# Kernel optimization log

Measured on AMD Instinct MI355X. Metric: run time of the kernel, lower is better.

## Reference

```python
import jax, jax.numpy as jnp
import numpy as np

HID = 256
VOC = 50257
N_E_SH = 2
N_E_SP = 2
N_MB = 4
B, S = 8, 512
LN_EPS = 1e-3  # keras LayerNormalization default epsilon
STD = 0.02


def setup_inputs() -> dict:
    key = jax.random.key(0)
    ks = jax.random.split(key, 10)
    x = jax.random.normal(ks[0], (B, S, HID), dtype=jnp.float32)
    # labels drawn in [1, VOC) so the `labels > 0` mask keeps every token (static shape)
    labels = jax.random.randint(ks[1], (B, S), 1, VOC, dtype=jnp.int32)
    xb = jax.random.randint(ks[2], (B, S), 0, N_MB + 1, dtype=jnp.int32)
    W_sh = jax.random.normal(ks[3], (N_E_SH, HID, HID), dtype=jnp.float32) * STD
    b_sh = jax.random.normal(ks[4], (N_E_SH, HID), dtype=jnp.float32) * STD
    W_sp = jax.random.normal(ks[5], (N_MB * N_E_SP, HID, HID), dtype=jnp.float32) * STD
    b_sp = jax.random.normal(ks[6], (N_MB * N_E_SP, HID), dtype=jnp.float32) * STD
    w_gates = jax.random.normal(ks[7], (N_MB, HID, N_E_SH + N_E_SP), dtype=jnp.float32) * STD
    vocab_bias = jax.random.normal(ks[8], (VOC,), dtype=jnp.float32) * STD
    emb = jax.random.normal(ks[9], (VOC, HID), dtype=jnp.float32) * STD  # tied_to.weights[0]
    ln_gamma = jnp.ones((HID,), dtype=jnp.float32)
    ln_beta = jnp.zeros((HID,), dtype=jnp.float32)
    return {"x": x, "labels": labels, "xb": xb, "W_sh": W_sh, "b_sh": b_sh,
            "W_sp": W_sp, "b_sp": b_sp, "w_gates": w_gates,
            "vocab_bias": vocab_bias, "emb": emb,
            "ln_gamma": ln_gamma, "ln_beta": ln_beta}


def _layernorm(h, gamma, beta):
    mu = jnp.mean(h, axis=-1, keepdims=True)
    var = jnp.mean(jnp.square(h - mu), axis=-1, keepdims=True)
    return gamma * (h - mu) * jax.lax.rsqrt(var + LN_EPS) + beta


def reference(x, labels, xb, W_sh, b_sh, W_sp, b_sp, w_gates, vocab_bias, emb, ln_gamma, ln_beta):
    xf = x.reshape(-1, HID)          # [N, H]
    lf = labels.reshape(-1)          # [N], all > 0 => mask gather is identity
    xbf = xb.reshape(-1)             # [N]

    # shared + branch-specific experts: [e, N, H]
    sh = jnp.einsum('nd,edh->enh', xf, W_sh) + b_sh[:, None, :]
    sp = jnp.einsum('nd,edh->enh', xf, W_sp) + b_sp[:, None, :]
    sp = sp.reshape(N_MB, N_E_SP, -1, HID)                       # [t, e_sp, N, H]
    sh_b = jnp.broadcast_to(sh[None], (N_MB, N_E_SH, sh.shape[1], HID))
    merge = jnp.concatenate([sh_b, sp], axis=1)                  # [t, e, N, H]

    gates = jax.nn.softmax(jnp.einsum('nd,tde->tne', xf, w_gates), axis=-1)  # [t, N, e]
    out = jnp.einsum('tend,tne->tnd', merge, gates)              # [t, N, H]

    outputs = jnp.concatenate([jnp.zeros_like(xf)[None], out], axis=0)  # [t+1, N, H]
    oh = jax.nn.one_hot(xbf, N_MB + 1, dtype=jnp.float32)        # [N, t+1]
    e_out = jnp.einsum('tnd,nt->nd', outputs, oh)                # [N, H]

    e_out = _layernorm(e_out, ln_gamma, ln_beta) + xf

    logits = e_out @ emb.T + vocab_bias                          # [N, VOC]
    logp = jax.nn.log_softmax(logits, axis=-1)
    loss = -jnp.take_along_axis(logp, lf[:, None], axis=-1)[:, 0]  # [N]
    prob = jnp.exp(logp)
    return prob, loss
```

## Files before the change

kernel.cpp:

```cpp
#include <hip/hip_runtime.h>

#define HID 256
#define VOC 50257
#define NTOK 4096
#define NCT3 393
#define CG 8
#define TN 128
#define LN_EPS 1e-3f
#define PROB_ELEMS 205852672

typedef __attribute__((ext_vector_type(8))) short bf16x8;
typedef __attribute__((ext_vector_type(4))) float f32x4;
typedef __attribute__((ext_vector_type(16))) float f32x16;

__device__ inline unsigned short f2bf(float f) {
    unsigned int u = __builtin_bit_cast(unsigned int, f);
    unsigned int r = u + 0x7FFFu + ((u >> 16) & 1u);
    return (unsigned short)(r >> 16);
}
__device__ inline float bf2f(unsigned short b) {
    unsigned int u = ((unsigned int)b) << 16;
    return __builtin_bit_cast(float, u);
}

__global__ void conv_f32_bf16(const float* __restrict__ src,
                              unsigned short* __restrict__ dst, int n4) {
    int i = blockIdx.x * blockDim.x + threadIdx.x;
    int stride = gridDim.x * blockDim.x;
    for (; i < n4; i += stride) {
        float4 v = reinterpret_cast<const float4*>(src)[i];
        ushort4 o;
        o.x = f2bf(v.x); o.y = f2bf(v.y); o.z = f2bf(v.z); o.w = f2bf(v.w);
        reinterpret_cast<ushort4*>(dst)[i] = o;
    }
}

__global__ __launch_bounds__(256) void wt_transpose(
    const float* __restrict__ Wsh, const float* __restrict__ Wsp,
    unsigned short* __restrict__ Wtbf) {
    __shared__ float t[64][65];
    int gcol0 = blockIdx.x * 64;
    int k0 = blockIdx.y * 64;
    int e = gcol0 >> 8, h0 = gcol0 & 255;
    const float* Wp = (e < 2) ? (Wsh + e * 65536) : (Wsp + (e - 2) * 65536);
    int tid = threadIdx.x;
#pragma unroll
    for (int i = 0; i < 16; ++i) {
        int id = tid + i * 256;
        int k = id >> 6, h = id & 63;
        t[k][h] = Wp[(k0 + k) * 256 + h0 + h];
    }
    __syncthreads();
#pragma unroll
    for (int i = 0; i < 4; ++i) {
        int id = tid + i * 256;
        int h = id >> 4, kq = id & 15;
        ushort4 o;
        o.x = f2bf(t[kq * 4 + 0][h]); o.y = f2bf(t[kq * 4 + 1][h]);
        o.z = f2bf(t[kq * 4 + 2][h]); o.w = f2bf(t[kq * 4 + 3][h]);
        *reinterpret_cast<ushort4*>(Wtbf + (size_t)(gcol0 + h) * 256 + k0 + kq * 4) = o;
    }
}

__global__ __launch_bounds__(256) void expert_gemm(
    const unsigned short* __restrict__ xbf,
    const unsigned short* __restrict__ Wtbf,
    const float* __restrict__ bsh, const float* __restrict__ bsp,
    float* __restrict__ cexp) {
    __shared__ unsigned short sA[64 * 256];
    __shared__ unsigned short sB[128 * 256];
    int bid = blockIdx.x;
    int rt = bid & 63;
    int ct = bid >> 6;
    int row0 = rt * 64, col0 = ct * 128;
    int tid = threadIdx.x;

#pragma unroll
    for (int i = 0; i < 8; ++i) {
        int id = tid + i * 256;
        int r = id >> 5, c = id & 31;
        bf16x8 v = *reinterpret_cast<const bf16x8*>(xbf + (row0 + r) * 256 + c * 8);
        *reinterpret_cast<bf16x8*>(sA + r * 256 + ((c ^ (r & 7)) * 8)) = v;
    }
#pragma unroll
    for (int i = 0; i < 16; ++i) {
        int id = tid + i * 256;
        int j = id >> 5, c = id & 31;
        bf16x8 v = *reinterpret_cast<const bf16x8*>(Wtbf + (size_t)(col0 + j) * 256 + c * 8);
        *reinterpret_cast<bf16x8*>(sB + j * 256 + ((c ^ (j & 7)) * 8)) = v;
    }
    __syncthreads();

    int lane = tid & 63, wave = tid >> 6;
    int wcol = wave * 32;
    int lrow = lane & 15, g = lane >> 4;
    f32x4 zero4 = {0.f, 0.f, 0.f, 0.f};
    f32x4 acc[4][2];
#pragma unroll
    for (int mf = 0; mf < 4; ++mf)
#pragma unroll
        for (int nf = 0; nf < 2; ++nf) acc[mf][nf] = zero4;

#pragma unroll
    for (int ks = 0; ks < 8; ++ks) {
        int kc = ks * 4 + g;
        bf16x8 a[4], b[2];
#pragma unroll
        for (int mf = 0; mf < 4; ++mf) {
            int r = mf * 16 + lrow;
            a[mf] = *reinterpret_cast<const bf16x8*>(sA + r * 256 + ((kc ^ (r & 7)) * 8));
        }
#pragma unroll
        for (int nf = 0; nf < 2; ++nf) {
            int j = wcol + nf * 16 + lrow;
            b[nf] = *reinterpret_cast<const bf16x8*>(sB + j * 256 + ((kc ^ (j & 7)) * 8));
        }
#pragma unroll
        for (int mf = 0; mf < 4; ++mf)
#pragma unroll
            for (int nf = 0; nf < 2; ++nf)
                acc[mf][nf] = __builtin_amdgcn_mfma_f32_16x16x32_bf16(a[mf], b[nf], acc[mf][nf], 0, 0, 0);
    }

#pragma unroll
    for (int nf = 0; nf < 2; ++nf) {
        int col = col0 + wcol + nf * 16 + lrow;
        int e = col >> 8, h = col & 255;
        float bias = (e < 2) ? bsh[e * 256 + h] : bsp[(e - 2) * 256 + h];
#pragma unroll
        for (int mf = 0; mf < 4; ++mf)
#pragma unroll
            for (int r = 0; r < 4; ++r) {
                int row = row0 + mf * 16 + g * 4 + r;
                cexp[(size_t)row * 2560 + col] = acc[mf][nf][r] + bias;
            }
    }
}

__global__ __launch_bounds__(256) void combine_ln(
    const float* __restrict__ x, const int* __restrict__ xb,
    const float* __restrict__ wg, const float* __restrict__ cexp,
    const float* __restrict__ gamma, const float* __restrict__ beta,
    unsigned short* __restrict__ ebf) {
    __shared__ float sx[256];
    __shared__ float sg[4];
    __shared__ float rs[4], rq[4];
    int n = blockIdx.x, h = threadIdx.x;
    float xv = x[n * 256 + h];
    sx[h] = xv;
    __syncthreads();
    int xbn = xb[n];
    float eo;
    if (xbn == 0) {
        eo = beta[h] + xv;
    } else {
        int t = xbn - 1;
        int wv = h >> 6, lane = h & 63;
        float p = 0.f;
        const float* wgt = wg + t * 1024;
#pragma unroll
        for (int i = 0; i < 4; ++i) {
            int d = lane * 4 + i;
            p += sx[d] * wgt[d * 4 + wv];
        }
#pragma unroll
        for (int off = 32; off; off >>= 1) p += __shfl_down(p, off);
        if (lane == 0) sg[wv] = p;
        __syncthreads();
        float g0 = sg[0], g1 = sg[1], g2 = sg[2], g3 = sg[3];
        float mx = fmaxf(fmaxf(g0, g1), fmaxf(g2, g3));
        float e0 = __expf(g0 - mx), e1 = __expf(g1 - mx);
        float e2 = __expf(g2 - mx), e3 = __expf(g3 - mx);
        float inv = 1.f / (e0 + e1 + e2 + e3);
        const float* cr = cexp + (size_t)n * 2560;
        float o = (e0 * cr[h] + e1 * cr[256 + h] +
                   e2 * cr[512 + t * 512 + h] + e3 * cr[768 + t * 512 + h]) * inv;
        float s = o, q = o * o;
#pragma unroll
        for (int off = 32; off; off >>= 1) { s += __shfl_down(s, off); q += __shfl_down(q, off); }
        if (lane == 0) { rs[wv] = s; rq[wv] = q; }
        __syncthreads();
        float mu = (rs[0] + rs[1] + rs[2] + rs[3]) * (1.f / 256.f);
        float ex2 = (rq[0] + rq[1] + rq[2] + rq[3]) * (1.f / 256.f);
        float var = ex2 - mu * mu;
        eo = gamma[h] * (o - mu) * rsqrtf(var + LN_EPS) + beta[h] + xv;
    }
    ebf[n * 256 + h] = f2bf(eo);
}

template <int PASS>
__global__ __launch_bounds__(512, 2) void big_gemm(
    const unsigned short* __restrict__ ebf,
    const unsigned short* __restrict__ embbf,
    const float* __restrict__ vbias,
    float* __restrict__ psum,
    const float* __restrict__ denom,
    float* __restrict__ prob) {
    __shared__ unsigned short sB[2][TN * 256];

    int bid = blockIdx.x;
    int rt = bid >> 3;
    int cg = bid & 7;
    int row0 = rt * 128;
    int tid = threadIdx.x;
    int wave = tid >> 6, lane = tid & 63;
    int l31 = lane & 31, hi = lane >> 5;
    int wr = wave >> 2, wc = wave & 3;
    int nmy = (NCT3 - cg + CG - 1) / CG;

    bf16x8 a[2][16];
    {
        const unsigned short* ab =
            ebf + (size_t)(row0 + wr * 64 + l31) * 256 + hi * 8;
#pragma unroll
        for (int mf = 0; mf < 2; ++mf)
#pragma unroll
            for (int ks = 0; ks < 16; ++ks)
                a[mf][ks] = *reinterpret_cast<const bf16x8*>(ab + mf * 32 * 256 + ks * 16);
    }

    auto stage = [&](int ct, int buf) {
        int col0 = ct * TN;
#pragma unroll
        for (int i = 0; i < 8; ++i) {
            int col = i * 16 + wave * 2 + hi;
            int gcol = col0 + col; if (gcol >= VOC) gcol = VOC - 1;
            const unsigned short* src =
                embbf + (size_t)gcol * 256 + ((l31 ^ (col & 7)) * 8);
            unsigned short* dst = (unsigned short*)sB[buf] + (size_t)(i * 512 + wave * 64) * 8;
            __builtin_amdgcn_global_load_lds(
                (const __attribute__((address_space(1))) void*)src,
                (__attribute__((address_space(3))) void*)dst, 16, 0, 0);
        }
    };

    stage(cg, 0);
    asm volatile("s_waitcnt vmcnt(0)" ::: "memory");
    __syncthreads();

    float invd[2][16];
    if (PASS == 1) {
#pragma unroll
        for (int mf = 0; mf < 2; ++mf)
#pragma unroll
            for (int r = 0; r < 16; ++r) {
                int row = row0 + wr * 64 + mf * 32 + (r & 3) + 8 * (r >> 2) + 4 * hi;
                invd[mf][r] = 1.f / denom[row];
            }
    }
    float es[2][16];
    if (PASS == 0) {
#pragma unroll
        for (int mf = 0; mf < 2; ++mf)
#pragma unroll
            for (int r = 0; r < 16; ++r) es[mf][r] = 0.f;
    }

    f32x16 zz = {0.f,0.f,0.f,0.f,0.f,0.f,0.f,0.f,0.f,0.f,0.f,0.f,0.f,0.f,0.f,0.f};

    for (int it = 0; it < nmy; ++it) {
        int ct = cg + it * CG;
        if (it + 1 < nmy) stage(ct + CG, (it + 1) & 1);

        int gc = ct * TN + wc * 32 + l31;
        float bvb;
        if (PASS == 0) bvb = (gc < VOC) ? vbias[gc] : -1e4f;
        else           bvb = vbias[(gc < VOC) ? gc : (VOC - 1)];

        const unsigned short* sBc = (const unsigned short*)sB[it & 1];
        int bcol = wc * 32 + l31;
        f32x16 c0 = zz, c1 = zz;
#pragma unroll
        for (int ks = 0; ks < 16; ++ks) {
            int kc = ks * 2 + hi;
            bf16x8 b = *reinterpret_cast<const bf16x8*>(
                sBc + bcol * 256 + ((kc ^ (bcol & 7)) * 8));
            c0 = __builtin_amdgcn_mfma_f32_32x32x16_bf16(a[0][ks], b, c0, 0, 0, 0);
            c1 = __builtin_amdgcn_mfma_f32_32x32x16_bf16(a[1][ks], b, c1, 0, 0, 0);
        }

        asm volatile("s_waitcnt vmcnt(0)" ::: "memory");
        __syncthreads();

        if (PASS == 0) {
#pragma unroll
            for (int r = 0; r < 16; ++r) {
                es[0][r] += __expf(c0[r] + bvb);
                es[1][r] += __expf(c1[r] + bvb);
            }
        } else {
            if (gc < VOC) {
#pragma unroll
                for (int r = 0; r < 16; ++r) {
                    int rowr = row0 + wr * 64 + (r & 3) + 8 * (r >> 2) + 4 * hi;
                    prob[(size_t)rowr * VOC + gc] = __expf(c0[r] + bvb) * invd[0][r];
                    prob[(size_t)(rowr + 32) * VOC + gc] = __expf(c1[r] + bvb) * invd[1][r];
                }
            }
        }
    }

    if (PASS == 0) {
#pragma unroll
        for (int mf = 0; mf < 2; ++mf)
#pragma unroll
            for (int r = 0; r < 16; ++r) {
                float v = es[mf][r];
#pragma unroll
                for (int off = 1; off < 32; off <<= 1) v += __shfl_xor(v, off);
                if (l31 == 0) {
                    int row = row0 + wr * 64 + mf * 32 + (r & 3) + 8 * (r >> 2) + 4 * hi;
                    psum[(size_t)row * 32 + cg * 4 + wc] = v;
                }
            }
    }
}

__global__ __launch_bounds__(64) void finalize_k(
    const float* __restrict__ psum,
    const unsigned short* __restrict__ ebf, const unsigned short* __restrict__ embbf,
    const float* __restrict__ vbias, const int* __restrict__ labels,
    float* __restrict__ denom, float* __restrict__ loss) {
    int n = blockIdx.x, lane = threadIdx.x;
    float s = (lane < 32) ? psum[(size_t)n * 32 + lane] : 0.f;
#pragma unroll
    for (int off = 1; off < 32; off <<= 1) s += __shfl_xor(s, off);
    int lf = labels[n];
    const unsigned short* ev = ebf + n * 256;
    const unsigned short* mv = embbf + (size_t)lf * 256;
    float p = 0.f;
#pragma unroll
    for (int i = 0; i < 4; ++i) p += bf2f(ev[lane * 4 + i]) * bf2f(mv[lane * 4 + i]);
#pragma unroll
    for (int off = 1; off < 64; off <<= 1) p += __shfl_xor(p, off);
    if (lane == 0) {
        denom[n] = s;
        loss[n] = logf(s) - (p + vbias[lf]);
    }
}

extern "C" void kernel_launch(void* const* d_in, const int* in_sizes, int n_in,
                              void* d_out, int out_size, void* d_ws, size_t ws_size,
                              hipStream_t stream) {
    const float* x      = (const float*)d_in[0];
    const int*   labels = (const int*)d_in[1];
    const int*   xb     = (const int*)d_in[2];
    const float* Wsh    = (const float*)d_in[3];
    const float* bsh    = (const float*)d_in[4];
    const float* Wsp    = (const float*)d_in[5];
    const float* bsp    = (const float*)d_in[6];
    const float* wg     = (const float*)d_in[7];
    const float* vbias  = (const float*)d_in[8];
    const float* emb    = (const float*)d_in[9];
    const float* gamma  = (const float*)d_in[10];
    const float* beta   = (const float*)d_in[11];

    char* ws = (char*)d_ws;
    unsigned short* xbf   = (unsigned short*)(ws + 0);
    unsigned short* embbf = (unsigned short*)(ws + 2097152);
    unsigned short* Wtbf  = (unsigned short*)(ws + 27828736);
    float* cexp           = (float*)(ws + 29360128);
    unsigned short* ebf   = (unsigned short*)(ws + 71303168);
    float* psum           = (float*)(ws + 73400320);
    float* denom          = (float*)(ws + 73924608);

    float* prob = (float*)d_out;
    float* loss = prob + PROB_ELEMS;

    conv_f32_bf16<<<dim3(512), dim3(256), 0, stream>>>(x, xbf, NTOK * HID / 4);
    conv_f32_bf16<<<dim3(2048), dim3(256), 0, stream>>>(emb, embbf, VOC * HID / 4);
    wt_transpose<<<dim3(40, 4), dim3(256), 0, stream>>>(Wsh, Wsp, Wtbf);
    expert_gemm<<<dim3(64 * 20), dim3(256), 0, stream>>>(xbf, Wtbf, bsh, bsp, cexp);
    combine_ln<<<dim3(NTOK), dim3(256), 0, stream>>>(x, xb, wg, cexp, gamma, beta, ebf);
    big_gemm<0><<<dim3(256), dim3(512), 0, stream>>>(ebf, embbf, vbias, psum, nullptr, nullptr);
    finalize_k<<<dim3(NTOK), dim3(64), 0, stream>>>(psum, ebf, embbf, vbias, labels, denom, loss);
    big_gemm<1><<<dim3(256), dim3(512), 0, stream>>>(ebf, embbf, vbias, nullptr, denom, prob);
}
```

Baseline: 540.1 us.

## Merge prep kernels, fuse x conversion into expert GEMM, shrink expert tile

Combines the emb bf16 conversion and the weight transpose into a single prep kernel, removing two launches. The expert GEMM now reads fp32 x directly and converts it to bf16 while staging into shared memory, which drops the separate x conversion pass. The expert GEMM column tile shrinks from 128 to 64, doubling the grid and cutting shared memory per block for better occupancy. In exchange each x tile is read and converted twice as many times, and each wave issues fewer MFMAs per A-fragment load.

Result: no change. 533.5 us (-1.2%).

```diff
diff --git a/kernel.cpp b/kernel.cpp
--- a/kernel.cpp
+++ b/kernel.cpp
@@ -23,67 +23,76 @@
     return __builtin_bit_cast(float, u);
 }
 
-__global__ void conv_f32_bf16(const float* __restrict__ src,
-                              unsigned short* __restrict__ dst, int n4) {
-    int i = blockIdx.x * blockDim.x + threadIdx.x;
-    int stride = gridDim.x * blockDim.x;
-    for (; i < n4; i += stride) {
-        float4 v = reinterpret_cast<const float4*>(src)[i];
-        ushort4 o;
-        o.x = f2bf(v.x); o.y = f2bf(v.y); o.z = f2bf(v.z); o.w = f2bf(v.w);
-        reinterpret_cast<ushort4*>(dst)[i] = o;
-    }
-}
-
-__global__ __launch_bounds__(256) void wt_transpose(
-    const float* __restrict__ Wsh, const float* __restrict__ Wsp,
-    unsigned short* __restrict__ Wtbf) {
+__global__ __launch_bounds__(256) void prep_kernel(
+    const float* __restrict__ emb, const float* __restrict__ Wsh,
+    const float* __restrict__ Wsp,
+    unsigned short* __restrict__ embbf, unsigned short* __restrict__ Wtbf) {
     __shared__ float t[64][65];
-    int gcol0 = blockIdx.x * 64;
-    int k0 = blockIdx.y * 64;
-    int e = gcol0 >> 8, h0 = gcol0 & 255;
-    const float* Wp = (e < 2) ? (Wsh + e * 65536) : (Wsp + (e - 2) * 65536);
     int tid = threadIdx.x;
-#pragma unroll
-    for (int i = 0; i < 16; ++i) {
-        int id = tid + i * 256;
-        int k = id >> 6, h = id & 63;
-        t[k][h] = Wp[(k0 + k) * 256 + h0 + h];
-    }
-    __syncthreads();
-#pragma unroll
-    for (int i = 0; i < 4; ++i) {
-        int id = tid + i * 256;
-        int h = id >> 4, kq = id & 15;
-        ushort4 o;
-        o.x = f2bf(t[kq * 4 + 0][h]); o.y = f2bf(t[kq * 4 + 1][h]);
-        o.z = f2bf(t[kq * 4 + 2][h]); o.w = f2bf(t[kq * 4 + 3][h]);
-        *reinterpret_cast<ushort4*>(Wtbf + (size_t)(gcol0 + h) * 256 + k0 + kq * 4) = o;
+    if (blockIdx.x < 160) {
+        int bx = blockIdx.x % 40, by = blockIdx.x / 40;
+        int gcol0 = bx * 64;
+        int k0 = by * 64;
+        int e = gcol0 >> 8, h0 = gcol0 & 255;
+        const float* Wp = (e < 2) ? (Wsh + e * 65536) : (Wsp + (e - 2) * 65536);
+#pragma unroll
+        for (int i = 0; i < 16; ++i) {
+            int id = tid + i * 256;
+            int k = id >> 6, h = id & 63;
+            t[k][h] = Wp[(k0 + k) * 256 + h0 + h];
+        }
+        __syncthreads();
+#pragma unroll
+        for (int i = 0; i < 4; ++i) {
+            int id = tid + i * 256;
+            int h = id >> 4, kq = id & 15;
+            ushort4 o;
+            o.x = f2bf(t[kq * 4 + 0][h]); o.y = f2bf(t[kq * 4 + 1][h]);
+            o.z = f2bf(t[kq * 4 + 2][h]); o.w = f2bf(t[kq * 4 + 3][h]);
+            *reinterpret_cast<ushort4*>(Wtbf + (size_t)(gcol0 + h) * 256 + k0 + kq * 4) = o;
+        }
+    } else {
+        const int n4 = VOC * HID / 4;
+        int i = (blockIdx.x - 160) * 256 + tid;
+        int stride = (gridDim.x - 160) * 256;
+        for (; i < n4; i += stride) {
+            float4 v = reinterpret_cast<const float4*>(emb)[i];
+            ushort4 o;
+            o.x = f2bf(v.x); o.y = f2bf(v.y); o.z = f2bf(v.z); o.w = f2bf(v.w);
+            reinterpret_cast<ushort4*>(embbf)[i] = o;
+        }
     }
 }
 
 __global__ __launch_bounds__(256) void expert_gemm(
-    const unsigned short* __restrict__ xbf,
+    const float* __restrict__ x,
     const unsigned short* __restrict__ Wtbf,
     const float* __restrict__ bsh, const float* __restrict__ bsp,
     float* __restrict__ cexp) {
     __shared__ unsigned short sA[64 * 256];
-    __shared__ unsigned short sB[128 * 256];
+    __shared__ unsigned short sB[64 * 256];
     int bid = blockIdx.x;
     int rt = bid & 63;
     int ct = bid >> 6;
-    int row0 = rt * 64, col0 = ct * 128;
+    int row0 = rt * 64, col0 = ct * 64;
     int tid = threadIdx.x;
 
 #pragma unroll
     for (int i = 0; i < 8; ++i) {
         int id = tid + i * 256;
         int r = id >> 5, c = id & 31;
-        bf16x8 v = *reinterpret_cast<const bf16x8*>(xbf + (row0 + r) * 256 + c * 8);
-        *reinterpret_cast<bf16x8*>(sA + r * 256 + ((c ^ (r & 7)) * 8)) = v;
-    }
-#pragma unroll
-    for (int i = 0; i < 16; ++i) {
+        const float* xr = x + (size_t)(row0 + r) * 256 + c * 8;
+        float4 v0 = *reinterpret_cast<const float4*>(xr);
+        float4 v1 = *reinterpret_cast<const float4*>(xr + 4);
+        bf16x8 o;
+        o[0] = (short)f2bf(v0.x); o[1] = (short)f2bf(v0.y);
+        o[2] = (short)f2bf(v0.z); o[3] = (short)f2bf(v0.w);
+        o[4] = (short)f2bf(v1.x); o[5] = (short)f2bf(v1.y);
+        o[6] = (short)f2bf(v1.z); o[7] = (short)f2bf(v1.w);
+        *reinterpret_cast<bf16x8*>(sA + r * 256 + ((c ^ (r & 7)) * 8)) = o;
+    }
+#pragma unroll
+    for (int i = 0; i < 8; ++i) {
         int id = tid + i * 256;
         int j = id >> 5, c = id & 31;
         bf16x8 v = *reinterpret_cast<const bf16x8*>(Wtbf + (size_t)(col0 + j) * 256 + c * 8);
@@ -92,39 +101,31 @@
     __syncthreads();
 
     int lane = tid & 63, wave = tid >> 6;
-    int wcol = wave * 32;
+    int wcol = wave * 16;
     int lrow = lane & 15, g = lane >> 4;
     f32x4 zero4 = {0.f, 0.f, 0.f, 0.f};
-    f32x4 acc[4][2];
-#pragma unroll
-    for (int mf = 0; mf < 4; ++mf)
-#pragma unroll
-        for (int nf = 0; nf < 2; ++nf) acc[mf][nf] = zero4;
+    f32x4 acc[4];
+#pragma unroll
+    for (int mf = 0; mf < 4; ++mf) acc[mf] = zero4;
 
 #pragma unroll
     for (int ks = 0; ks < 8; ++ks) {
         int kc = ks * 4 + g;
-        bf16x8 a[4], b[2];
+        int j = wcol + lrow;
+        bf16x8 b = *reinterpret_cast<const bf16x8*>(sB + j * 256 + ((kc ^ (j & 7)) * 8));
+        bf16x8 a[4];
 #pragma unroll
         for (int mf = 0; mf < 4; ++mf) {
             int r = mf * 16 + lrow;
             a[mf] = *reinterpret_cast<const bf16x8*>(sA + r * 256 + ((kc ^ (r & 7)) * 8));
         }
 #pragma unroll
-        for (int nf = 0; nf < 2; ++nf) {
-            int j = wcol + nf * 16 + lrow;
-            b[nf] = *reinterpret_cast<const bf16x8*>(sB + j * 256 + ((kc ^ (j & 7)) * 8));
-        }
-#pragma unroll
         for (int mf = 0; mf < 4; ++mf)
-#pragma unroll
-            for (int nf = 0; nf < 2; ++nf)
-                acc[mf][nf] = __builtin_amdgcn_mfma_f32_16x16x32_bf16(a[mf], b[nf], acc[mf][nf], 0, 0, 0);
-    }
-
-#pragma unroll
-    for (int nf = 0; nf < 2; ++nf) {
-        int col = col0 + wcol + nf * 16 + lrow;
+            acc[mf] = __builtin_amdgcn_mfma_f32_16x16x32_bf16(a[mf], b, acc[mf], 0, 0, 0);
+    }
+
+    {
+        int col = col0 + wcol + lrow;
         int e = col >> 8, h = col & 255;
         float bias = (e < 2) ? bsh[e * 256 + h] : bsp[(e - 2) * 256 + h];
 #pragma unroll
@@ -132,7 +133,7 @@
 #pragma unroll
             for (int r = 0; r < 4; ++r) {
                 int row = row0 + mf * 16 + g * 4 + r;
-                cexp[(size_t)row * 2560 + col] = acc[mf][nf][r] + bias;
+                cexp[(size_t)row * 2560 + col] = acc[mf][r] + bias;
             }
     }
 }
@@ -356,7 +357,6 @@
     const float* beta   = (const float*)d_in[11];
 
     char* ws = (char*)d_ws;
-    unsigned short* xbf   = (unsigned short*)(ws + 0);
     unsigned short* embbf = (unsigned short*)(ws + 2097152);
     unsigned short* Wtbf  = (unsigned short*)(ws + 27828736);
     float* cexp           = (float*)(ws + 29360128);
@@ -367,10 +367,8 @@
     float* prob = (float*)d_out;
     float* loss = prob + PROB_ELEMS;
 
-    conv_f32_bf16<<<dim3(512), dim3(256), 0, stream>>>(x, xbf, NTOK * HID / 4);
-    conv_f32_bf16<<<dim3(2048), dim3(256), 0, stream>>>(emb, embbf, VOC * HID / 4);
-    wt_transpose<<<dim3(40, 4), dim3(256), 0, stream>>>(Wsh, Wsp, Wtbf);
-    expert_gemm<<<dim3(64 * 20), dim3(256), 0, stream>>>(xbf, Wtbf, bsh, bsp, cexp);
+    prep_kernel<<<dim3(2208), dim3(256), 0, stream>>>(emb, Wsh, Wsp, embbf, Wtbf);
+    expert_gemm<<<dim3(64 * 40), dim3(256), 0, stream>>>(x, Wtbf, bsh, bsp, cexp);
     combine_ln<<<dim3(NTOK), dim3(256), 0, stream>>>(x, xb, wg, cexp, gamma, beta, ebf);
     big_gemm<0><<<dim3(256), dim3(512), 0, stream>>>(ebf, embbf, vbias, psum, nullptr, nullptr);
     finalize_k<<<dim3(NTOK), dim3(64), 0, stream>>>(psum, ebf, embbf, vbias, labels, denom, loss);
```
